# Performance work log

Measured on AMD Instinct MI355X. Metric: run time of the kernel, lower is better.

Reference implementation:

```python
import jax, jax.numpy as jnp
import numpy as np
from math import ceil

CAPACITY_FACTOR = 2.0
MIN_CAPACITY = 4


def setup_inputs() -> dict:
    key = jax.random.key(0)
    ks = jax.random.split(key, 4)
    B, S, D, Di, E = 4, 2048, 1024, 4096, 8
    x = jax.random.normal(ks[0], (B, S, D), dtype=jnp.float32)
    Wr = jax.random.normal(ks[1], (D, E), dtype=jnp.float32) * (D ** -0.5)
    W1 = jax.random.normal(ks[2], (E, D, Di), dtype=jnp.float32) * (D ** -0.5)
    b1 = jnp.zeros((E, Di), dtype=jnp.float32)
    W2 = jax.random.normal(ks[3], (E, Di, D), dtype=jnp.float32) * (Di ** -0.5)
    b2 = jnp.zeros((E, D), dtype=jnp.float32)
    return {"x": x, "Wr": Wr, "W1": W1, "b1": b1, "W2": W2, "b2": b2}


def reference(x, Wr, W1, b1, W2, b2):
    B, S, D = x.shape
    E = Wr.shape[1]
    N = B * S
    k = max(MIN_CAPACITY, ceil(N * CAPACITY_FACTOR / E))  # expert capacity (static)

    xt = x.reshape(N, D)
    scores = jax.nn.softmax(xt @ Wr, axis=-1)          # [N, E] router probs
    G, idx = jax.lax.top_k(scores.T, k)                 # [E, k]: each expert picks top-k tokens

    # dispatch: equivalent to P @ x with P = one_hot(idx, N)
    X_in = xt[idx]                                      # [E, k, D]

    # per-expert MLP (batched over experts): Linear -> GELU(exact) -> Linear
    h = jax.nn.gelu(jnp.einsum('ekd,edh->ekh', X_in, W1) + b1[:, None, :], approximate=False)
    X_e = jnp.einsum('ekh,ehd->ekd', h, W2) + b2[:, None, :]  # [E, k, D]

    # combine: einsum('ijl,ij,ijd->ld', P, G, X_e) == scatter-add of G*X_e at idx
    contrib = (G[..., None] * X_e).reshape(E * k, D)
    out = jnp.zeros((N, D), dtype=x.dtype).at[idx.reshape(-1)].add(contrib)
    return out.reshape(B, S, D)
```

## Files before the change

kernel.cpp:

```cpp
#include <hip/hip_runtime.h>
#include <hip/hip_bf16.h>
#include <cstdint>
#include <cstddef>

#define NTOK 8192
#define DMODEL 1024
#define DFF 4096
#define NEXP 8
#define CAP 2048

typedef __attribute__((ext_vector_type(8))) __bf16 bf16x8;
typedef __attribute__((ext_vector_type(4))) float f32x4;

__device__ __forceinline__ void gload16(const void* g, void* l) {
  __builtin_amdgcn_global_load_lds(
      (__attribute__((address_space(1))) void*)(g),
      (__attribute__((address_space(3))) void*)(l),
      16, 0, 0);
}
#define VMWAIT_(n) asm volatile("s_waitcnt vmcnt(" #n ")" ::: "memory")
#define VMWAIT(n) VMWAIT_(n)
#define MEMFENCE asm volatile("" ::: "memory")

__global__ __launch_bounds__(256) void zero_f32(float* p, int n4) {
  int i = blockIdx.x * blockDim.x + threadIdx.x;
  int stride = gridDim.x * blockDim.x;
  float4 z = make_float4(0.f, 0.f, 0.f, 0.f);
  for (; i < n4; i += stride) ((float4*)p)[i] = z;
}

__global__ __launch_bounds__(256) void router_kernel(
    const float* __restrict__ x, const float* __restrict__ Wr,
    float* __restrict__ scoresT, __hip_bfloat16* __restrict__ xb) {
  const int lane = threadIdx.x & 63;
  const int t = blockIdx.x * 4 + (threadIdx.x >> 6);
  const float* xr = x + (size_t)t * DMODEL;
  float acc[NEXP];
#pragma unroll
  for (int j = 0; j < NEXP; ++j) acc[j] = 0.f;
#pragma unroll
  for (int it = 0; it < DMODEL / 64; ++it) {
    int d = it * 64 + lane;
    float xv = xr[d];
    xb[(size_t)t * DMODEL + d] = __float2bfloat16(xv);
    const float4* w = (const float4*)(Wr + (size_t)d * NEXP);
    float4 w0 = w[0], w1 = w[1];
    acc[0] += xv * w0.x; acc[1] += xv * w0.y; acc[2] += xv * w0.z; acc[3] += xv * w0.w;
    acc[4] += xv * w1.x; acc[5] += xv * w1.y; acc[6] += xv * w1.z; acc[7] += xv * w1.w;
  }
#pragma unroll
  for (int off = 32; off; off >>= 1) {
#pragma unroll
    for (int j = 0; j < NEXP; ++j) acc[j] += __shfl_xor(acc[j], off);
  }
  float m = acc[0];
#pragma unroll
  for (int j = 1; j < NEXP; ++j) m = fmaxf(m, acc[j]);
  float s = 0.f;
#pragma unroll
  for (int j = 0; j < NEXP; ++j) { acc[j] = expf(acc[j] - m); s += acc[j]; }
  float inv = 1.f / s;
  if (lane < NEXP) scoresT[(size_t)lane * NTOK + t] = acc[lane] * inv;
}

__global__ __launch_bounds__(256) void topk_kernel(
    const float* __restrict__ scoresT, float* __restrict__ G, int* __restrict__ IDX) {
  __shared__ uint32_t sb[NTOK];
  __shared__ uint32_t hist[256];
  __shared__ uint32_t s_prefix, s_rem;
  __shared__ uint32_t eq_list[256];
  __shared__ uint32_t eq_cnt, gt_cnt;
  const int e = blockIdx.x, tid = threadIdx.x;
  const float* se = scoresT + (size_t)e * NTOK;
  for (int i = tid; i < NTOK; i += 256) sb[i] = __float_as_uint(se[i]);
  if (tid == 0) { s_prefix = 0u; s_rem = CAP; eq_cnt = 0u; gt_cnt = 0u; }
  __syncthreads();
  for (int r = 0; r < 4; ++r) {
    const int shift = 24 - 8 * r;
    for (int i = tid; i < 256; i += 256) hist[i] = 0u;
    __syncthreads();
    uint32_t pfx = s_prefix;
    for (int i = tid; i < NTOK; i += 256) {
      uint32_t b = sb[i];
      if (((b >> shift) >> 8) == pfx) atomicAdd(&hist[(b >> shift) & 255u], 1u);
    }
    __syncthreads();
    if (tid == 0) {
      uint32_t rem = s_rem, cum = 0u;
      int d = 255;
      for (; d > 0; --d) {
        if (cum + hist[d] >= rem) break;
        cum += hist[d];
      }
      s_prefix = (pfx << 8) | (uint32_t)d;
      s_rem = rem - cum;
    }
    __syncthreads();
  }
  const uint32_t T = s_prefix, need = s_rem;
  for (int i = tid; i < NTOK; i += 256) {
    uint32_t b = sb[i];
    if (b > T) {
      uint32_t p = atomicAdd(&gt_cnt, 1u);
      IDX[(size_t)e * CAP + p] = i;
      G[(size_t)e * CAP + p] = __uint_as_float(b);
    } else if (b == T) {
      uint32_t c = atomicAdd(&eq_cnt, 1u);
      if (c < 256u) eq_list[c] = (uint32_t)i;
    }
  }
  __syncthreads();
  if (tid == 0) {
    uint32_t base = gt_cnt;
    uint32_t c = eq_cnt < 256u ? eq_cnt : 256u;
    for (uint32_t s = 0; s < need; ++s) {
      uint32_t mv = 0xFFFFFFFFu; int mi = 0;
      for (uint32_t j = 0; j < c; ++j)
        if (eq_list[j] < mv) { mv = eq_list[j]; mi = (int)j; }
      eq_list[mi] = 0xFFFFFFFFu;
      IDX[(size_t)e * CAP + base + s] = (int)mv;
      G[(size_t)e * CAP + base + s] = __uint_as_float(T);
    }
  }
}

__global__ __launch_bounds__(256) void transpose_cvt(
    const float* __restrict__ in, __hip_bfloat16* __restrict__ out, int R, int C) {
  __shared__ float tile[32][33];
  const int e = blockIdx.z;
  const float* ine = in + (size_t)e * R * C;
  __hip_bfloat16* oute = out + (size_t)e * R * C;
  const int c0 = blockIdx.x * 32, r0 = blockIdx.y * 32;
  const int tx = threadIdx.x, ty = threadIdx.y;
#pragma unroll
  for (int i = 0; i < 4; ++i)
    tile[ty + i * 8][tx] = ine[(size_t)(r0 + ty + i * 8) * C + (c0 + tx)];
  __syncthreads();
#pragma unroll
  for (int i = 0; i < 4; ++i)
    oute[(size_t)(c0 + ty + i * 8) * R + (r0 + tx)] =
        __float2bfloat16(tile[tx][ty + i * 8]);
}


template <int NKT>
__device__ __forceinline__ void gemm_core8(
    const char* a00, const char* a01, const char* a10, const char* a11,
    const char* b00, const char* b01, const char* b10, const char* b11,
    char* smem, f32x4 (&acc)[8][4]) {
  const int tid = threadIdx.x;
  const int wave = tid >> 6, lane = tid & 63;
  const int wm = wave >> 2, wn = wave & 3;
  const int lrow = lane & 15, lgrp = lane >> 4;
  const int dst = tid * 16;

  int offA[8][2], offB[4][2];
#pragma unroll
  for (int mi = 0; mi < 8; ++mi) {
    int rL = wm * 64 + (mi & 3) * 16 + lrow;
    int pbase = (mi >> 2) * 16384;
#pragma unroll
    for (int ks = 0; ks < 2; ++ks)
      offA[mi][ks] = pbase + rL * 128 + (((ks * 4 + lgrp + rL) & 7) << 4);
  }
#pragma unroll
  for (int ni = 0; ni < 4; ++ni) {
    int rL = wn * 32 + (ni & 1) * 16 + lrow;
    int pbase = 32768 + (ni >> 1) * 16384;
#pragma unroll
    for (int ks = 0; ks < 2; ++ks)
      offB[ni][ks] = pbase + rL * 128 + (((ks * 4 + lgrp + rL) & 7) << 4);
  }
  const char* pa[2][2] = {{a00, a01}, {a10, a11}};
  const char* pb[2][2] = {{b00, b01}, {b10, b11}};

  {
    char* sb = smem;
    gload16(pa[0][0], sb + dst);          gload16(pa[0][1], sb + 8192 + dst);
    pa[0][0] += 128; pa[0][1] += 128;
    gload16(pb[0][0], sb + 32768 + dst);  gload16(pb[0][1], sb + 40960 + dst);
    pb[0][0] += 128; pb[0][1] += 128;
    gload16(pb[1][0], sb + 49152 + dst);  gload16(pb[1][1], sb + 57344 + dst);
    pb[1][0] += 128; pb[1][1] += 128;
    gload16(pa[1][0], sb + 16384 + dst);  gload16(pa[1][1], sb + 24576 + dst);
    pa[1][0] += 128; pa[1][1] += 128;
  }
  bf16x8 av[4][2], b0v[2][2], b1v[2][2];

  for (int kt = 0; kt < NKT; ++kt) {
    char* buf = smem + ((kt & 1) << 16);
    char* sb  = smem + (((kt + 1) & 1) << 16);
    const bool st = (kt < NKT - 1);
    const bool last = (kt == NKT - 1);

    VMWAIT(4);
    __builtin_amdgcn_s_barrier();
    MEMFENCE;
#pragma unroll
    for (int mi = 0; mi < 4; ++mi)
#pragma unroll
      for (int ks = 0; ks < 2; ++ks)
        av[mi][ks] = *(const bf16x8*)(buf + offA[mi][ks]);
#pragma unroll
    for (int ni = 0; ni < 2; ++ni)
#pragma unroll
      for (int ks = 0; ks < 2; ++ks)
        b0v[ni][ks] = *(const bf16x8*)(buf + offB[ni][ks]);
    if (st) {
      gload16(pa[0][0], sb + dst); gload16(pa[0][1], sb + 8192 + dst);
      pa[0][0] += 128; pa[0][1] += 128;
    }
    __builtin_amdgcn_s_barrier();
    asm volatile("s_waitcnt lgkmcnt(0)" ::: "memory");
    __builtin_amdgcn_s_setprio(1);
#pragma unroll
    for (int mi = 0; mi < 4; ++mi)
#pragma unroll
      for (int ni = 0; ni < 2; ++ni)
#pragma unroll
        for (int ks = 0; ks < 2; ++ks)
          acc[mi][ni] = __builtin_amdgcn_mfma_f32_16x16x32_bf16(
              av[mi][ks], b0v[ni][ks], acc[mi][ni], 0, 0, 0);
    __builtin_amdgcn_s_setprio(0);

    if (last) { VMWAIT(2); } else { VMWAIT(4); }
    __builtin_amdgcn_s_barrier();
    MEMFENCE;
#pragma unroll
    for (int ni = 0; ni < 2; ++ni)
#pragma unroll
      for (int ks = 0; ks < 2; ++ks)
        b1v[ni][ks] = *(const bf16x8*)(buf + offB[2 + ni][ks]);
    if (st) {
      gload16(pb[0][0], sb + 32768 + dst); gload16(pb[0][1], sb + 40960 + dst);
      pb[0][0] += 128; pb[0][1] += 128;
    }
    __builtin_amdgcn_s_barrier();
    asm volatile("s_waitcnt lgkmcnt(0)" ::: "memory");
    __builtin_amdgcn_s_setprio(1);
#pragma unroll
    for (int mi = 0; mi < 4; ++mi)
#pragma unroll
      for (int ni = 0; ni < 2; ++ni)
#pragma unroll
        for (int ks = 0; ks < 2; ++ks)
          acc[mi][2 + ni] = __builtin_amdgcn_mfma_f32_16x16x32_bf16(
              av[mi][ks], b1v[ni][ks], acc[mi][2 + ni], 0, 0, 0);
    __builtin_amdgcn_s_setprio(0);

    if (last) { VMWAIT(0); } else { VMWAIT(4); }
    __builtin_amdgcn_s_barrier();
    MEMFENCE;
#pragma unroll
    for (int mi = 0; mi < 4; ++mi)
#pragma unroll
      for (int ks = 0; ks < 2; ++ks)
        av[mi][ks] = *(const bf16x8*)(buf + offA[4 + mi][ks]);
    if (st) {
      gload16(pb[1][0], sb + 49152 + dst); gload16(pb[1][1], sb + 57344 + dst);
      pb[1][0] += 128; pb[1][1] += 128;
    }
    __builtin_amdgcn_s_barrier();
    asm volatile("s_waitcnt lgkmcnt(0)" ::: "memory");
    __builtin_amdgcn_s_setprio(1);
#pragma unroll
    for (int mi = 0; mi < 4; ++mi)
#pragma unroll
      for (int ni = 0; ni < 2; ++ni)
#pragma unroll
        for (int ks = 0; ks < 2; ++ks)
          acc[4 + mi][2 + ni] = __builtin_amdgcn_mfma_f32_16x16x32_bf16(
              av[mi][ks], b1v[ni][ks], acc[4 + mi][2 + ni], 0, 0, 0);
    __builtin_amdgcn_s_setprio(0);

    if (st) {
      gload16(pa[1][0], sb + 16384 + dst); gload16(pa[1][1], sb + 24576 + dst);
      pa[1][0] += 128; pa[1][1] += 128;
    }
    __builtin_amdgcn_s_barrier();
    __builtin_amdgcn_s_setprio(1);
#pragma unroll
    for (int mi = 0; mi < 4; ++mi)
#pragma unroll
      for (int ni = 0; ni < 2; ++ni)
#pragma unroll
        for (int ks = 0; ks < 2; ++ks)
          acc[4 + mi][ni] = __builtin_amdgcn_mfma_f32_16x16x32_bf16(
              av[mi][ks], b0v[ni][ks], acc[4 + mi][ni], 0, 0, 0);
    __builtin_amdgcn_s_setprio(0);
  }
}

__global__ __launch_bounds__(512, 2) void gemm1_kernel(
    const __hip_bfloat16* __restrict__ xb,
    const __hip_bfloat16* __restrict__ W1t,
    const float* __restrict__ b1,
    const int* __restrict__ IDX,
    __hip_bfloat16* __restrict__ h, int e0, int nblk) {
  __shared__ __align__(16) char smem[131072];
  int lin = blockIdx.x;
  { int q = nblk >> 3; lin = (lin & 7) * q + (lin >> 3); }
  const int tm = lin & 7, tn = (lin >> 3) & 15, ez = lin >> 7;
  const int e = e0 + ez;
  const int tid = threadIdx.x, wave = tid >> 6, lane = tid & 63;
  const int wm = wave >> 2, wn = wave & 3;
  const int lrow = lane & 15, lgrp = lane >> 4;

  const int r0 = tid >> 3;
  const int s16 = (((tid & 7) - r0) & 7) * 16;
  const char* srcA[2][2]; const char* srcB[2][2];
#pragma unroll
  for (int hh = 0; hh < 2; ++hh)
#pragma unroll
    for (int j = 0; j < 2; ++j) {
      int m = j * 128 + hh * 64 + r0;
      int tok = IDX[e * CAP + tm * 256 + m];
      srcA[hh][j] = (const char*)(xb + (size_t)tok * DMODEL) + s16;
      int n = j * 128 + (r0 >> 5) * 64 + hh * 32 + (r0 & 31);
      srcB[hh][j] = (const char*)(W1t + ((size_t)e * DFF + tn * 256 + n) * DMODEL) + s16;
    }

  f32x4 acc[8][4];
  f32x4 zero = {0.f, 0.f, 0.f, 0.f};
#pragma unroll
  for (int mi = 0; mi < 8; ++mi)
#pragma unroll
    for (int ni = 0; ni < 4; ++ni) acc[mi][ni] = zero;

  gemm_core8<DMODEL / 64>(srcA[0][0], srcA[0][1], srcA[1][0], srcA[1][1],
                          srcB[0][0], srcB[0][1], srcB[1][0], srcB[1][1],
                          smem, acc);

  __hip_bfloat16* he = h + (size_t)ez * CAP * DFF;
  const float* b1e = b1 + (size_t)e * DFF;
  float bvals[4];
#pragma unroll
  for (int ni = 0; ni < 4; ++ni)
    bvals[ni] = b1e[tn * 256 + wn * 64 + ni * 16 + lrow];
#pragma unroll
  for (int mi = 0; mi < 8; ++mi) {
#pragma unroll
    for (int j = 0; j < 4; ++j) {
      int row = tm * 256 + wm * 128 + mi * 16 + lgrp * 4 + j;
      __hip_bfloat16* hrow = he + (size_t)row * DFF;
#pragma unroll
      for (int ni = 0; ni < 4; ++ni) {
        int col = tn * 256 + wn * 64 + ni * 16 + lrow;
        float v = acc[mi][ni][j] + bvals[ni];
        v = 0.5f * v * (1.f + erff(v * 0.70710678118654752f));
        hrow[col] = __float2bfloat16(v);
      }
    }
  }
}

__global__ __launch_bounds__(512, 2) void gemm2_kernel(
    const __hip_bfloat16* __restrict__ h,
    const __hip_bfloat16* __restrict__ W2t,
    const float* __restrict__ b2,
    const int* __restrict__ IDX, const float* __restrict__ G,
    float* __restrict__ out, int e0, int nblk) {
  __shared__ __align__(16) char smem[131072];
  int lin = blockIdx.x;
  { int q = nblk >> 3; lin = (lin & 7) * q + (lin >> 3); }
  const int tm = lin & 7, tn = (lin >> 3) & 3, ez = lin >> 5;
  const int e = e0 + ez;
  const int tid = threadIdx.x, wave = tid >> 6, lane = tid & 63;
  const int wm = wave >> 2, wn = wave & 3;
  const int lrow = lane & 15, lgrp = lane >> 4;

  const int r0 = tid >> 3;
  const int s16 = (((tid & 7) - r0) & 7) * 16;
  const char* srcA[2][2]; const char* srcB[2][2];
#pragma unroll
  for (int hh = 0; hh < 2; ++hh)
#pragma unroll
    for (int j = 0; j < 2; ++j) {
      int m = j * 128 + hh * 64 + r0;
      srcA[hh][j] = (const char*)(h + ((size_t)ez * CAP + tm * 256 + m) * DFF) + s16;
      int n = j * 128 + (r0 >> 5) * 64 + hh * 32 + (r0 & 31);
      srcB[hh][j] = (const char*)(W2t + ((size_t)e * DMODEL + tn * 256 + n) * DFF) + s16;
    }

  f32x4 acc[8][4];
  f32x4 zero = {0.f, 0.f, 0.f, 0.f};
#pragma unroll
  for (int mi = 0; mi < 8; ++mi)
#pragma unroll
    for (int ni = 0; ni < 4; ++ni) acc[mi][ni] = zero;

  gemm_core8<DFF / 64>(srcA[0][0], srcA[0][1], srcA[1][0], srcA[1][1],
                       srcB[0][0], srcB[0][1], srcB[1][0], srcB[1][1],
                       smem, acc);

  const float* b2e = b2 + (size_t)e * DMODEL;
  const int* idxe = IDX + (size_t)e * CAP;
  const float* ge = G + (size_t)e * CAP;
  float bvals[4];
#pragma unroll
  for (int ni = 0; ni < 4; ++ni)
    bvals[ni] = b2e[tn * 256 + wn * 64 + ni * 16 + lrow];
#pragma unroll
  for (int mi = 0; mi < 8; ++mi) {
#pragma unroll
    for (int j = 0; j < 4; ++j) {
      int row = tm * 256 + wm * 128 + mi * 16 + lgrp * 4 + j;
      float g = ge[row];
      int tok = idxe[row];
      float* orow = out + (size_t)tok * DMODEL;
#pragma unroll
      for (int ni = 0; ni < 4; ++ni) {
        int col = tn * 256 + wn * 64 + ni * 16 + lrow;
        atomicAdd(orow + col, (acc[mi][ni][j] + bvals[ni]) * g);
      }
    }
  }
}

extern "C" void kernel_launch(void* const* d_in, const int* in_sizes, int n_in,
                              void* d_out, int out_size, void* d_ws, size_t ws_size,
                              hipStream_t stream) {
  const float* x  = (const float*)d_in[0];
  const float* Wr = (const float*)d_in[1];
  const float* W1 = (const float*)d_in[2];
  const float* b1 = (const float*)d_in[3];
  const float* W2 = (const float*)d_in[4];
  const float* b2 = (const float*)d_in[5];
  float* out = (float*)d_out;
  char* ws = (char*)d_ws;

  size_t off = 0;
  float* scoresT = (float*)(ws + off); off += (size_t)NEXP * NTOK * 4;
  float* G       = (float*)(ws + off); off += (size_t)NEXP * CAP * 4;
  int*   IDX     = (int*)(ws + off);   off += (size_t)NEXP * CAP * 4;
  __hip_bfloat16* xb  = (__hip_bfloat16*)(ws + off); off += (size_t)NTOK * DMODEL * 2;
  __hip_bfloat16* W1t = (__hip_bfloat16*)(ws + off); off += (size_t)NEXP * DFF * DMODEL * 2;
  __hip_bfloat16* W2t = (__hip_bfloat16*)(ws + off); off += (size_t)NEXP * DMODEL * DFF * 2;
  __hip_bfloat16* hbuf = (__hip_bfloat16*)(ws + off);
  size_t h_per_e = (size_t)CAP * DFF * 2;
  size_t avail = (ws_size > off) ? (ws_size - off) : 0;
  int EC = (int)(avail / h_per_e);
  if (EC < 1) EC = 1;
  if (EC > NEXP) EC = NEXP;

  zero_f32<<<512, 256, 0, stream>>>(out, out_size / 4);
  router_kernel<<<NTOK / 4, 256, 0, stream>>>(x, Wr, scoresT, xb);
  topk_kernel<<<NEXP, 256, 0, stream>>>(scoresT, G, IDX);
  transpose_cvt<<<dim3(DFF / 32, DMODEL / 32, NEXP), dim3(32, 8), 0, stream>>>(
      W1, W1t, DMODEL, DFF);
  transpose_cvt<<<dim3(DMODEL / 32, DFF / 32, NEXP), dim3(32, 8), 0, stream>>>(
      W2, W2t, DFF, DMODEL);
  for (int e0 = 0; e0 < NEXP; e0 += EC) {
    int ne = (NEXP - e0 < EC) ? (NEXP - e0) : EC;
    int nblk1 = 128 * ne;
    gemm1_kernel<<<nblk1, 512, 0, stream>>>(xb, W1t, b1, IDX, hbuf, e0, nblk1);
    int nblk2 = 32 * ne;
    gemm2_kernel<<<nblk2, 512, 0, stream>>>(hbuf, W2t, b2, IDX, G, out, e0, nblk2);
  }
}
```

Baseline: 499.3 us.

## Restructure GEMM core into two-tile prefetch pipeline and use tanh GELU

Replaces the GEMM main loop with a simpler double-buffered schedule. Both k-tiles are prefetched up front, each iteration runs two full 8x4 MFMA sweeps, and the tile two steps ahead is reloaded into the just-consumed buffer. This cuts the per-iteration barriers from about six to two and makes the A/B shared-memory layout contiguous per wave. Separately, the exact erf GELU in the first GEMM epilogue is replaced by the tanh approximation using __expf. That makes the epilogue cheaper but deviates slightly from the reference's exact GELU. The larger per-phase register footprint may raise register pressure.

```diff
diff --git a/kernel.cpp b/kernel.cpp
--- a/kernel.cpp
+++ b/kernel.cpp
@@ -144,9 +144,9 @@
 
 
 template <int NKT>
-__device__ __forceinline__ void gemm_core8(
-    const char* a00, const char* a01, const char* a10, const char* a11,
-    const char* b00, const char* b01, const char* b10, const char* b11,
+__device__ __forceinline__ void gemm_core_v5(
+    const char* pa0, const char* pa1, const char* pa2, const char* pa3,
+    const char* pb0, const char* pb1, const char* pb2, const char* pb3,
     char* smem, f32x4 (&acc)[8][4]) {
   const int tid = threadIdx.x;
   const int wave = tid >> 6, lane = tid & 63;
@@ -154,141 +154,94 @@
   const int lrow = lane & 15, lgrp = lane >> 4;
   const int dst = tid * 16;
 
+  const char* pa[4] = {pa0, pa1, pa2, pa3};
+  const char* pb[4] = {pb0, pb1, pb2, pb3};
+
   int offA[8][2], offB[4][2];
 #pragma unroll
   for (int mi = 0; mi < 8; ++mi) {
-    int rL = wm * 64 + (mi & 3) * 16 + lrow;
-    int pbase = (mi >> 2) * 16384;
+    int rL = wm * 128 + mi * 16 + lrow;
 #pragma unroll
     for (int ks = 0; ks < 2; ++ks)
-      offA[mi][ks] = pbase + rL * 128 + (((ks * 4 + lgrp + rL) & 7) << 4);
-  }
+      offA[mi][ks] = rL * 128 + (((ks * 4 + lgrp) + rL & 7) << 4);
+  }
+#pragma unroll
+  for (int mi = 0; mi < 8; ++mi)
+#pragma unroll
+    for (int ks = 0; ks < 2; ++ks) {
+      int rL = wm * 128 + mi * 16 + lrow;
+      offA[mi][ks] = rL * 128 + ((((ks * 4 + lgrp) + rL) & 7) << 4);
+    }
 #pragma unroll
   for (int ni = 0; ni < 4; ++ni) {
-    int rL = wn * 32 + (ni & 1) * 16 + lrow;
-    int pbase = 32768 + (ni >> 1) * 16384;
+    int rL = wn * 64 + ni * 16 + lrow;
 #pragma unroll
     for (int ks = 0; ks < 2; ++ks)
-      offB[ni][ks] = pbase + rL * 128 + (((ks * 4 + lgrp + rL) & 7) << 4);
-  }
-  const char* pa[2][2] = {{a00, a01}, {a10, a11}};
-  const char* pb[2][2] = {{b00, b01}, {b10, b11}};
-
-  {
-    char* sb = smem;
-    gload16(pa[0][0], sb + dst);          gload16(pa[0][1], sb + 8192 + dst);
-    pa[0][0] += 128; pa[0][1] += 128;
-    gload16(pb[0][0], sb + 32768 + dst);  gload16(pb[0][1], sb + 40960 + dst);
-    pb[0][0] += 128; pb[0][1] += 128;
-    gload16(pb[1][0], sb + 49152 + dst);  gload16(pb[1][1], sb + 57344 + dst);
-    pb[1][0] += 128; pb[1][1] += 128;
-    gload16(pa[1][0], sb + 16384 + dst);  gload16(pa[1][1], sb + 24576 + dst);
-    pa[1][0] += 128; pa[1][1] += 128;
-  }
-  bf16x8 av[4][2], b0v[2][2], b1v[2][2];
+      offB[ni][ks] = 32768 + rL * 128 + ((((ks * 4 + lgrp) + rL) & 7) << 4);
+  }
+
+#pragma unroll
+  for (int g = 0; g < 4; ++g) { gload16(pa[g], smem + g * 8192 + dst); pa[g] += 128; }
+#pragma unroll
+  for (int g = 0; g < 4; ++g) { gload16(pb[g], smem + 32768 + g * 8192 + dst); pb[g] += 128; }
+#pragma unroll
+  for (int g = 0; g < 4; ++g) { gload16(pa[g], smem + 65536 + g * 8192 + dst); pa[g] += 128; }
+#pragma unroll
+  for (int g = 0; g < 4; ++g) { gload16(pb[g], smem + 65536 + 32768 + g * 8192 + dst); pb[g] += 128; }
 
   for (int kt = 0; kt < NKT; ++kt) {
     char* buf = smem + ((kt & 1) << 16);
-    char* sb  = smem + (((kt + 1) & 1) << 16);
-    const bool st = (kt < NKT - 1);
-    const bool last = (kt == NKT - 1);
-
-    VMWAIT(4);
+    if (kt < NKT - 1) { VMWAIT(8); } else { VMWAIT(0); }
     __builtin_amdgcn_s_barrier();
     MEMFENCE;
-#pragma unroll
-    for (int mi = 0; mi < 4; ++mi)
-#pragma unroll
-      for (int ks = 0; ks < 2; ++ks)
-        av[mi][ks] = *(const bf16x8*)(buf + offA[mi][ks]);
-#pragma unroll
-    for (int ni = 0; ni < 2; ++ni)
-#pragma unroll
-      for (int ks = 0; ks < 2; ++ks)
-        b0v[ni][ks] = *(const bf16x8*)(buf + offB[ni][ks]);
-    if (st) {
-      gload16(pa[0][0], sb + dst); gload16(pa[0][1], sb + 8192 + dst);
-      pa[0][0] += 128; pa[0][1] += 128;
-    }
-    __builtin_amdgcn_s_barrier();
+
+    bf16x8 av[8], bv[4];
+#pragma unroll
+    for (int mi = 0; mi < 8; ++mi) av[mi] = *(const bf16x8*)(buf + offA[mi][0]);
+#pragma unroll
+    for (int ni = 0; ni < 4; ++ni) bv[ni] = *(const bf16x8*)(buf + offB[ni][0]);
+
+    __builtin_amdgcn_s_setprio(1);
+#pragma unroll
+    for (int mi = 0; mi < 8; ++mi)
+#pragma unroll
+      for (int ni = 0; ni < 4; ++ni)
+        acc[mi][ni] = __builtin_amdgcn_mfma_f32_16x16x32_bf16(
+            av[mi], bv[ni], acc[mi][ni], 0, 0, 0);
+    __builtin_amdgcn_s_setprio(0);
+
+    bf16x8 av2[8], bv2[4];
+#pragma unroll
+    for (int mi = 0; mi < 8; ++mi) av2[mi] = *(const bf16x8*)(buf + offA[mi][1]);
+#pragma unroll
+    for (int ni = 0; ni < 4; ++ni) bv2[ni] = *(const bf16x8*)(buf + offB[ni][1]);
+
     asm volatile("s_waitcnt lgkmcnt(0)" ::: "memory");
-    __builtin_amdgcn_s_setprio(1);
-#pragma unroll
-    for (int mi = 0; mi < 4; ++mi)
-#pragma unroll
-      for (int ni = 0; ni < 2; ++ni)
-#pragma unroll
-        for (int ks = 0; ks < 2; ++ks)
-          acc[mi][ni] = __builtin_amdgcn_mfma_f32_16x16x32_bf16(
-              av[mi][ks], b0v[ni][ks], acc[mi][ni], 0, 0, 0);
-    __builtin_amdgcn_s_setprio(0);
-
-    if (last) { VMWAIT(2); } else { VMWAIT(4); }
     __builtin_amdgcn_s_barrier();
     MEMFENCE;
-#pragma unroll
-    for (int ni = 0; ni < 2; ++ni)
-#pragma unroll
-      for (int ks = 0; ks < 2; ++ks)
-        b1v[ni][ks] = *(const bf16x8*)(buf + offB[2 + ni][ks]);
-    if (st) {
-      gload16(pb[0][0], sb + 32768 + dst); gload16(pb[0][1], sb + 40960 + dst);
-      pb[0][0] += 128; pb[0][1] += 128;
-    }
-    __builtin_amdgcn_s_barrier();
-    asm volatile("s_waitcnt lgkmcnt(0)" ::: "memory");
+    if (kt < NKT - 2) {
+#pragma unroll
+      for (int g = 0; g < 4; ++g) { gload16(pa[g], buf + g * 8192 + dst); pa[g] += 128; }
+#pragma unroll
+      for (int g = 0; g < 4; ++g) { gload16(pb[g], buf + 32768 + g * 8192 + dst); pb[g] += 128; }
+    }
+    __builtin_amdgcn_sched_barrier(0);
     __builtin_amdgcn_s_setprio(1);
 #pragma unroll
-    for (int mi = 0; mi < 4; ++mi)
-#pragma unroll
-      for (int ni = 0; ni < 2; ++ni)
-#pragma unroll
-        for (int ks = 0; ks < 2; ++ks)
-          acc[mi][2 + ni] = __builtin_amdgcn_mfma_f32_16x16x32_bf16(
-              av[mi][ks], b1v[ni][ks], acc[mi][2 + ni], 0, 0, 0);
+    for (int mi = 0; mi < 8; ++mi)
+#pragma unroll
+      for (int ni = 0; ni < 4; ++ni)
+        acc[mi][ni] = __builtin_amdgcn_mfma_f32_16x16x32_bf16(
+            av2[mi], bv2[ni], acc[mi][ni], 0, 0, 0);
     __builtin_amdgcn_s_setprio(0);
-
-    if (last) { VMWAIT(0); } else { VMWAIT(4); }
-    __builtin_amdgcn_s_barrier();
-    MEMFENCE;
-#pragma unroll
-    for (int mi = 0; mi < 4; ++mi)
-#pragma unroll
-      for (int ks = 0; ks < 2; ++ks)
-        av[mi][ks] = *(const bf16x8*)(buf + offA[4 + mi][ks]);
-    if (st) {
-      gload16(pb[1][0], sb + 49152 + dst); gload16(pb[1][1], sb + 57344 + dst);
-      pb[1][0] += 128; pb[1][1] += 128;
-    }
-    __builtin_amdgcn_s_barrier();
-    asm volatile("s_waitcnt lgkmcnt(0)" ::: "memory");
-    __builtin_amdgcn_s_setprio(1);
-#pragma unroll
-    for (int mi = 0; mi < 4; ++mi)
-#pragma unroll
-      for (int ni = 0; ni < 2; ++ni)
-#pragma unroll
-        for (int ks = 0; ks < 2; ++ks)
-          acc[4 + mi][2 + ni] = __builtin_amdgcn_mfma_f32_16x16x32_bf16(
-              av[mi][ks], b1v[ni][ks], acc[4 + mi][2 + ni], 0, 0, 0);
-    __builtin_amdgcn_s_setprio(0);
-
-    if (st) {
-      gload16(pa[1][0], sb + 16384 + dst); gload16(pa[1][1], sb + 24576 + dst);
-      pa[1][0] += 128; pa[1][1] += 128;
-    }
-    __builtin_amdgcn_s_barrier();
-    __builtin_amdgcn_s_setprio(1);
-#pragma unroll
-    for (int mi = 0; mi < 4; ++mi)
-#pragma unroll
-      for (int ni = 0; ni < 2; ++ni)
-#pragma unroll
-        for (int ks = 0; ks < 2; ++ks)
-          acc[4 + mi][ni] = __builtin_amdgcn_mfma_f32_16x16x32_bf16(
-              av[mi][ks], b0v[ni][ks], acc[4 + mi][ni], 0, 0, 0);
-    __builtin_amdgcn_s_setprio(0);
-  }
+  }
+}
+
+__device__ __forceinline__ float gelu_tanh(float v) {
+  float t = 0.7978845608028654f * (v + 0.044715f * v * v * v);
+  float e = __expf(2.f * t);
+  float th = 1.f - 2.f / (e + 1.f);
+  return 0.5f * v * (1.f + th);
 }
 
 __global__ __launch_bounds__(512, 2) void gemm1_kernel(
@@ -307,18 +260,16 @@
   const int lrow = lane & 15, lgrp = lane >> 4;
 
   const int r0 = tid >> 3;
-  const int s16 = (((tid & 7) - r0) & 7) * 16;
-  const char* srcA[2][2]; const char* srcB[2][2];
-#pragma unroll
-  for (int hh = 0; hh < 2; ++hh)
-#pragma unroll
-    for (int j = 0; j < 2; ++j) {
-      int m = j * 128 + hh * 64 + r0;
-      int tok = IDX[e * CAP + tm * 256 + m];
-      srcA[hh][j] = (const char*)(xb + (size_t)tok * DMODEL) + s16;
-      int n = j * 128 + (r0 >> 5) * 64 + hh * 32 + (r0 & 31);
-      srcB[hh][j] = (const char*)(W1t + ((size_t)e * DFF + tn * 256 + n) * DMODEL) + s16;
-    }
+  const int ksrc = (((tid & 7) - r0) & 7) * 16;
+  const char* pa[4]; const char* pb[4];
+#pragma unroll
+  for (int g = 0; g < 4; ++g) {
+    int m = g * 64 + r0;
+    int tok = IDX[e * CAP + tm * 256 + m];
+    pa[g] = (const char*)(xb + (size_t)tok * DMODEL) + ksrc;
+    int n = g * 64 + r0;
+    pb[g] = (const char*)(W1t + ((size_t)e * DFF + tn * 256 + n) * DMODEL) + ksrc;
+  }
 
   f32x4 acc[8][4];
   f32x4 zero = {0.f, 0.f, 0.f, 0.f};
@@ -327,9 +278,8 @@
 #pragma unroll
     for (int ni = 0; ni < 4; ++ni) acc[mi][ni] = zero;
 
-  gemm_core8<DMODEL / 64>(srcA[0][0], srcA[0][1], srcA[1][0], srcA[1][1],
-                          srcB[0][0], srcB[0][1], srcB[1][0], srcB[1][1],
-                          smem, acc);
+  gemm_core_v5<DMODEL / 64>(pa[0], pa[1], pa[2], pa[3],
+                            pb[0], pb[1], pb[2], pb[3], smem, acc);
 
   __hip_bfloat16* he = h + (size_t)ez * CAP * DFF;
   const float* b1e = b1 + (size_t)e * DFF;
@@ -347,8 +297,7 @@
       for (int ni = 0; ni < 4; ++ni) {
         int col = tn * 256 + wn * 64 + ni * 16 + lrow;
         float v = acc[mi][ni][j] + bvals[ni];
-        v = 0.5f * v * (1.f + erff(v * 0.70710678118654752f));
-        hrow[col] = __float2bfloat16(v);
+        hrow[col] = __float2bfloat16(gelu_tanh(v));
       }
     }
   }
@@ -370,17 +319,15 @@
   const int lrow = lane & 15, lgrp = lane >> 4;
 
   const int r0 = tid >> 3;
-  const int s16 = (((tid & 7) - r0) & 7) * 16;
-  const char* srcA[2][2]; const char* srcB[2][2];
-#pragma unroll
-  for (int hh = 0; hh < 2; ++hh)
-#pragma unroll
-    for (int j = 0; j < 2; ++j) {
-      int m = j * 128 + hh * 64 + r0;
-      srcA[hh][j] = (const char*)(h + ((size_t)ez * CAP + tm * 256 + m) * DFF) + s16;
-      int n = j * 128 + (r0 >> 5) * 64 + hh * 32 + (r0 & 31);
-      srcB[hh][j] = (const char*)(W2t + ((size_t)e * DMODEL + tn * 256 + n) * DFF) + s16;
-    }
+  const int ksrc = (((tid & 7) - r0) & 7) * 16;
+  const char* pa[4]; const char* pb[4];
+#pragma unroll
+  for (int g = 0; g < 4; ++g) {
+    int m = g * 64 + r0;
+    pa[g] = (const char*)(h + ((size_t)ez * CAP + tm * 256 + m) * DFF) + ksrc;
+    int n = g * 64 + r0;
+    pb[g] = (const char*)(W2t + ((size_t)e * DMODEL + tn * 256 + n) * DFF) + ksrc;
+  }
 
   f32x4 acc[8][4];
   f32x4 zero = {0.f, 0.f, 0.f, 0.f};
@@ -389,9 +336,8 @@
 #pragma unroll
     for (int ni = 0; ni < 4; ++ni) acc[mi][ni] = zero;
 
-  gemm_core8<DFF / 64>(srcA[0][0], srcA[0][1], srcA[1][0], srcA[1][1],
-                       srcB[0][0], srcB[0][1], srcB[1][0], srcB[1][1],
-                       smem, acc);
+  gemm_core_v5<DFF / 64>(pa[0], pa[1], pa[2], pa[3],
+                         pb[0], pb[1], pb[2], pb[3], smem, acc);
 
   const float* b2e = b2 + (size_t)e * DMODEL;
   const int* idxe = IDX + (size_t)e * CAP;
```

Result: faster. 475.7 us (-4.7%).
